# Kernel tuning notes

Measured on AMD Instinct MI355X. Metric: run time of the kernel, lower is better.

## Reference

```python
import jax, jax.numpy as jnp
import numpy as np

N_NODES = 100000
N_EDGES = 1000000
NODE_DIM = 64
HIDDEN_DIM = 128


def setup_inputs() -> dict:
    key = jax.random.key(0)
    ks = jax.random.split(key, 9)
    x = jax.random.normal(ks[0], (N_NODES, NODE_DIM), dtype=jnp.float32)
    y = jax.random.normal(ks[1], (N_NODES, NODE_DIM), dtype=jnp.float32)
    edge_index = jax.random.randint(ks[2], (2, N_EDGES), 0, N_NODES, dtype=jnp.int64)
    pos_x = jax.random.normal(ks[3], (N_NODES, 3), dtype=jnp.float32)
    pos_y = jax.random.normal(ks[4], (N_NODES, 3), dtype=jnp.float32)
    in_dim = NODE_DIM * 2 + 1
    # Kaiming-uniform-ish init like torch Linear
    lim1 = 1.0 / np.sqrt(in_dim)
    lim2 = 1.0 / np.sqrt(HIDDEN_DIM)
    W1 = jax.random.uniform(ks[5], (in_dim, HIDDEN_DIM), jnp.float32, -lim1, lim1)
    b1 = jax.random.uniform(ks[6], (HIDDEN_DIM,), jnp.float32, -lim1, lim1)
    W2 = jax.random.uniform(ks[7], (HIDDEN_DIM, 1), jnp.float32, -lim2, lim2)
    b2 = jax.random.uniform(ks[8], (1,), jnp.float32, -lim2, lim2)
    return {"x": x, "y": y, "edge_index": edge_index, "pos_x": pos_x,
            "pos_y": pos_y, "W1": W1, "b1": b1, "W2": W2, "b2": b2}


def reference(x, y, edge_index, pos_x, pos_y, W1, b1, W2, b2):
    src = edge_index[0]
    dst = edge_index[1]
    # per-edge euclidean distance between endpoint positions  [E]
    d = pos_x[src] - pos_y[dst]                      # [E, 3]
    dist = jnp.sqrt(jnp.sum(d * d, axis=1))          # [E]
    # gather + concat: [E, node_dim*2 + 1]
    mlp_in = jnp.concatenate([x[src], y[dst], dist[:, None]], axis=1)
    h = jax.nn.relu(mlp_in @ W1 + b1)                # [E, hidden]
    out = jax.nn.relu(h @ W2 + b2)                   # [E, 1]
    return out
```

## Files before the change

kernel.cpp:

```cpp
#include <hip/hip_runtime.h>
#include <hip/hip_bf16.h>


constexpr int NDIM  = 64;
constexpr int HID   = 128;
constexpr int KPAD  = 136;

typedef __attribute__((ext_vector_type(8))) short  short8;
typedef __attribute__((ext_vector_type(4))) int    int4v;
typedef __attribute__((ext_vector_type(4))) float  floatx4;

__device__ __forceinline__ short f2bf(float f) {
    union { __hip_bfloat16 h; short s; } cv;
    cv.h = __float2bfloat16(f);
    return cv.s;
}

__device__ __forceinline__ int pack2(float a, float b) {
    union { __hip_bfloat162 h; int u; } cv;
    cv.h = __float22bfloat162_rn(float2{a, b});
    return cv.u;
}

__device__ __forceinline__ short8 make_afrag(const float* rp) {
    const floatx4 f0 = *reinterpret_cast<const floatx4*>(rp);
    const floatx4 f1 = *reinterpret_cast<const floatx4*>(rp + 4);
    union { int4v i; short8 s8; } cv;
    cv.i.x = pack2(f0.x, f0.y);
    cv.i.y = pack2(f0.z, f0.w);
    cv.i.z = pack2(f1.x, f1.y);
    cv.i.w = pack2(f1.z, f1.w);
    return cv.s8;
}

__global__ __launch_bounds__(256, 3) void edge_mlp_kernel(
    const float* __restrict__ x, const float* __restrict__ y,
    const int*  __restrict__ ei, const float* __restrict__ px,
    const float* __restrict__ py, const float* __restrict__ W1,
    const float* __restrict__ b1, const float* __restrict__ W2,
    const float* __restrict__ b2, float* __restrict__ out, int E)
{
    __shared__ __align__(16) short Wt[HID * KPAD];

    const int tid = threadIdx.x;

    for (int base = 0; base < HID * HID; base += 256 * 8) {
        float f[8];
#pragma unroll
        for (int u = 0; u < 8; ++u) f[u] = W1[base + u * 256 + tid];
#pragma unroll
        for (int u = 0; u < 8; ++u) {
            int i = base + u * 256 + tid;
            Wt[(i & 127) * KPAD + (i >> 7)] = f2bf(f[u]);
        }
    }
    if (tid < HID) {
        const int n = tid;
        Wt[n * KPAD + 128] = f2bf(W1[128 * HID + n]);
        Wt[n * KPAD + 129] = f2bf(b1[n]);
#pragma unroll
        for (int j = 130; j < 136; ++j) Wt[n * KPAD + j] = 0;
    }
    __syncthreads();

    const int lane = tid & 63;
    const int wave = tid >> 6;
    const int quad = lane >> 4;
    const int lm   = lane & 15;

    float w2v[8];
#pragma unroll
    for (int t = 0; t < 8; ++t) w2v[t] = W2[t * 16 + lm];
    const float b2s = b2[0];

    const int* __restrict__ srcp = ei;
    const int* __restrict__ dstp = ei + E;

    const int sel5 = (quad == 0) ? 128 : 0;

    const int ntiles = (E + 127) / 128;
    for (int tile = blockIdx.x; tile < ntiles; tile += gridDim.x) {
        const int mb = tile * 128 + wave * 32;
        int m0 = mb + lm;       if (m0 >= E) m0 = E - 1;
        int m1 = mb + 16 + lm;  if (m1 >= E) m1 = E - 1;
        const int src0 = srcp[m0], dst0 = dstp[m0];
        const int src1 = srcp[m1], dst1 = dstp[m1];

        const float dx0 = px[src0 * 3 + 0] - py[dst0 * 3 + 0];
        const float dy0 = px[src0 * 3 + 1] - py[dst0 * 3 + 1];
        const float dz0 = px[src0 * 3 + 2] - py[dst0 * 3 + 2];
        const float dist0 = sqrtf(dx0 * dx0 + dy0 * dy0 + dz0 * dz0);
        const float dx1 = px[src1 * 3 + 0] - py[dst1 * 3 + 0];
        const float dy1 = px[src1 * 3 + 1] - py[dst1 * 3 + 1];
        const float dz1 = px[src1 * 3 + 2] - py[dst1 * 3 + 2];
        const float dist1 = sqrtf(dx1 * dx1 + dy1 * dy1 + dz1 * dz1);

        short8 fa[4], fb[4];
#pragma unroll
        for (int s = 0; s < 4; ++s) {
            const int kk = s * 32 + quad * 8;
            fa[s] = make_afrag((s < 2) ? (x + src0 * NDIM + kk) : (y + dst0 * NDIM + (kk - 64)));
            fb[s] = make_afrag((s < 2) ? (x + src1 * NDIM + kk) : (y + dst1 * NDIM + (kk - 64)));
        }
        short8 fa4, fb4;
        {
            union { int4v i; short8 s8; } ca, cb;
            const int d0 = (quad == 0) ? pack2(dist0, 1.0f) : 0;
            const int d1 = (quad == 0) ? pack2(dist1, 1.0f) : 0;
            ca.i = int4v{d0, 0, 0, 0};
            cb.i = int4v{d1, 0, 0, 0};
            fa4 = ca.s8; fb4 = cb.s8;
        }

        floatx4 accA[8], accB[8];
#pragma unroll
        for (int t = 0; t < 8; ++t) {
            accA[t] = floatx4{0.f, 0.f, 0.f, 0.f};
            accB[t] = floatx4{0.f, 0.f, 0.f, 0.f};
        }

        int zoff = 0;
        asm volatile("" : "+v"(zoff));
        const short* wr  = Wt + zoff + lm * KPAD + quad * 8;
        const short* wr5 = Wt + zoff + lm * KPAD + sel5;

#pragma unroll
        for (int t = 0; t < 8; ++t) {
            const short* base = wr + t * (16 * KPAD);
            const short8 bg0 = *reinterpret_cast<const short8*>(base);
            const short8 bg1 = *reinterpret_cast<const short8*>(base + 32);
            const short8 bg2 = *reinterpret_cast<const short8*>(base + 64);
            const short8 bg3 = *reinterpret_cast<const short8*>(base + 96);
            const short8 bg4 = *reinterpret_cast<const short8*>(wr5 + t * (16 * KPAD));
            accA[t] = __builtin_amdgcn_mfma_f32_16x16x32_bf16(fa[0], bg0, accA[t], 0, 0, 0);
            accB[t] = __builtin_amdgcn_mfma_f32_16x16x32_bf16(fb[0], bg0, accB[t], 0, 0, 0);
            accA[t] = __builtin_amdgcn_mfma_f32_16x16x32_bf16(fa[1], bg1, accA[t], 0, 0, 0);
            accB[t] = __builtin_amdgcn_mfma_f32_16x16x32_bf16(fb[1], bg1, accB[t], 0, 0, 0);
            accA[t] = __builtin_amdgcn_mfma_f32_16x16x32_bf16(fa[2], bg2, accA[t], 0, 0, 0);
            accB[t] = __builtin_amdgcn_mfma_f32_16x16x32_bf16(fb[2], bg2, accB[t], 0, 0, 0);
            accA[t] = __builtin_amdgcn_mfma_f32_16x16x32_bf16(fa[3], bg3, accA[t], 0, 0, 0);
            accB[t] = __builtin_amdgcn_mfma_f32_16x16x32_bf16(fb[3], bg3, accB[t], 0, 0, 0);
            accA[t] = __builtin_amdgcn_mfma_f32_16x16x32_bf16(fa4,  bg4, accA[t], 0, 0, 0);
            accB[t] = __builtin_amdgcn_mfma_f32_16x16x32_bf16(fb4,  bg4, accB[t], 0, 0, 0);
        }

        float p0 = 0.f, p1 = 0.f, p2 = 0.f, p3 = 0.f;
        float q0 = 0.f, q1 = 0.f, q2 = 0.f, q3 = 0.f;
#pragma unroll
        for (int t = 0; t < 8; ++t) {
            p0 += fmaxf(accA[t][0], 0.f) * w2v[t];
            p1 += fmaxf(accA[t][1], 0.f) * w2v[t];
            p2 += fmaxf(accA[t][2], 0.f) * w2v[t];
            p3 += fmaxf(accA[t][3], 0.f) * w2v[t];
            q0 += fmaxf(accB[t][0], 0.f) * w2v[t];
            q1 += fmaxf(accB[t][1], 0.f) * w2v[t];
            q2 += fmaxf(accB[t][2], 0.f) * w2v[t];
            q3 += fmaxf(accB[t][3], 0.f) * w2v[t];
        }
#pragma unroll
        for (int off = 1; off < 16; off <<= 1) {
            p0 += __shfl_xor(p0, off, 64);
            p1 += __shfl_xor(p1, off, 64);
            p2 += __shfl_xor(p2, off, 64);
            p3 += __shfl_xor(p3, off, 64);
            q0 += __shfl_xor(q0, off, 64);
            q1 += __shfl_xor(q1, off, 64);
            q2 += __shfl_xor(q2, off, 64);
            q3 += __shfl_xor(q3, off, 64);
        }
        if (lm < 4) {
            const float vA = (lm == 0) ? p0 : (lm == 1) ? p1 : (lm == 2) ? p2 : p3;
            const float vB = (lm == 0) ? q0 : (lm == 1) ? q1 : (lm == 2) ? q2 : q3;
            const int eA = mb + quad * 4 + lm;
            const int eB = mb + 16 + quad * 4 + lm;
            if (eA < E) out[eA] = fmaxf(vA + b2s, 0.f);
            if (eB < E) out[eB] = fmaxf(vB + b2s, 0.f);
        }
    }
}

extern "C" void kernel_launch(void* const* d_in, const int* in_sizes, int n_in,
                              void* d_out, int out_size, void* d_ws, size_t ws_size,
                              hipStream_t stream)
{
    const float* x  = (const float*)d_in[0];
    const float* y  = (const float*)d_in[1];
    const int*   ei = (const int*)  d_in[2];
    const float* px = (const float*)d_in[3];
    const float* py = (const float*)d_in[4];
    const float* W1 = (const float*)d_in[5];
    const float* b1 = (const float*)d_in[6];
    const float* W2 = (const float*)d_in[7];
    const float* b2 = (const float*)d_in[8];
    float* out = (float*)d_out;
    const int E = in_sizes[2] / 2;

    edge_mlp_kernel<<<dim3(768), dim3(256), 0, stream>>>(
        x, y, ei, px, py, W1, b1, W2, b2, out, E);
}
```

Before: 192.4 us.

## Pre-convert node features to bf16 in workspace before gathered edge MLP

Adds a conversion kernel that writes bf16 copies of x and y into the workspace, then the edge kernel gathers 16-byte bf16 rows instead of 32-byte fp32 rows and skips the per-edge conversion. This targets the random-gather bandwidth, which dominates with a million edges. The cost is an extra pass over 51 MB of node features and a second launch each call, with a fallback to the old path when the workspace is too small.

```diff
diff --git a/kernel.cpp b/kernel.cpp
--- a/kernel.cpp
+++ b/kernel.cpp
@@ -22,7 +22,7 @@
     return cv.u;
 }
 
-__device__ __forceinline__ short8 make_afrag(const float* rp) {
+__device__ __forceinline__ short8 make_afrag_f32(const float* rp) {
     const floatx4 f0 = *reinterpret_cast<const floatx4*>(rp);
     const floatx4 f1 = *reinterpret_cast<const floatx4*>(rp + 4);
     union { int4v i; short8 s8; } cv;
@@ -33,8 +33,36 @@
     return cv.s8;
 }
 
+__global__ __launch_bounds__(256) void cvt_kernel(
+    const float* __restrict__ xin, const float* __restrict__ yin,
+    short* __restrict__ xb, short* __restrict__ yb, int nfl)
+{
+    const int stride = gridDim.x * blockDim.x;
+    const int n8 = nfl >> 3;
+    for (int i = blockIdx.x * blockDim.x + threadIdx.x; i < n8; i += stride) {
+        {
+            const floatx4 f0 = *reinterpret_cast<const floatx4*>(xin + i * 8);
+            const floatx4 f1 = *reinterpret_cast<const floatx4*>(xin + i * 8 + 4);
+            union { int4v v; short8 s; } c;
+            c.v.x = pack2(f0.x, f0.y); c.v.y = pack2(f0.z, f0.w);
+            c.v.z = pack2(f1.x, f1.y); c.v.w = pack2(f1.z, f1.w);
+            *reinterpret_cast<short8*>(xb + i * 8) = c.s;
+        }
+        {
+            const floatx4 f0 = *reinterpret_cast<const floatx4*>(yin + i * 8);
+            const floatx4 f1 = *reinterpret_cast<const floatx4*>(yin + i * 8 + 4);
+            union { int4v v; short8 s; } c;
+            c.v.x = pack2(f0.x, f0.y); c.v.y = pack2(f0.z, f0.w);
+            c.v.z = pack2(f1.x, f1.y); c.v.w = pack2(f1.z, f1.w);
+            *reinterpret_cast<short8*>(yb + i * 8) = c.s;
+        }
+    }
+}
+
+template <bool BF16GATHER>
 __global__ __launch_bounds__(256, 3) void edge_mlp_kernel(
     const float* __restrict__ x, const float* __restrict__ y,
+    const short* __restrict__ xb, const short* __restrict__ yb,
     const int*  __restrict__ ei, const float* __restrict__ px,
     const float* __restrict__ py, const float* __restrict__ W1,
     const float* __restrict__ b1, const float* __restrict__ W2,
@@ -99,8 +127,19 @@
 #pragma unroll
         for (int s = 0; s < 4; ++s) {
             const int kk = s * 32 + quad * 8;
-            fa[s] = make_afrag((s < 2) ? (x + src0 * NDIM + kk) : (y + dst0 * NDIM + (kk - 64)));
-            fb[s] = make_afrag((s < 2) ? (x + src1 * NDIM + kk) : (y + dst1 * NDIM + (kk - 64)));
+            if (BF16GATHER) {
+                const short* pa = (s < 2) ? (xb + src0 * NDIM + kk)
+                                          : (yb + dst0 * NDIM + (kk - 64));
+                const short* pb = (s < 2) ? (xb + src1 * NDIM + kk)
+                                          : (yb + dst1 * NDIM + (kk - 64));
+                fa[s] = *reinterpret_cast<const short8*>(pa);
+                fb[s] = *reinterpret_cast<const short8*>(pb);
+            } else {
+                fa[s] = make_afrag_f32((s < 2) ? (x + src0 * NDIM + kk)
+                                               : (y + dst0 * NDIM + (kk - 64)));
+                fb[s] = make_afrag_f32((s < 2) ? (x + src1 * NDIM + kk)
+                                               : (y + dst1 * NDIM + (kk - 64)));
+            }
         }
         short8 fa4, fb4;
         {
@@ -194,7 +233,17 @@
     const float* b2 = (const float*)d_in[8];
     float* out = (float*)d_out;
     const int E = in_sizes[2] / 2;
-
-    edge_mlp_kernel<<<dim3(768), dim3(256), 0, stream>>>(
-        x, y, ei, px, py, W1, b1, W2, b2, out, E);
-}
+    const int nnode_elems = in_sizes[0];
+
+    const size_t need = (size_t)nnode_elems * 2 * sizeof(short);
+    if (ws_size >= need) {
+        short* xb = (short*)d_ws;
+        short* yb = xb + nnode_elems;
+        cvt_kernel<<<dim3(1024), dim3(256), 0, stream>>>(x, y, xb, yb, nnode_elems);
+        edge_mlp_kernel<true><<<dim3(768), dim3(256), 0, stream>>>(
+            x, y, xb, yb, ei, px, py, W1, b1, W2, b2, out, E);
+    } else {
+        edge_mlp_kernel<false><<<dim3(768), dim3(256), 0, stream>>>(
+            x, y, nullptr, nullptr, ei, px, py, W1, b1, W2, b2, out, E);
+    }
+}
```

Result: faster. 162.6 us (-15.5%).
